# Kernel tuning notes

Hardware: AMD Instinct MI355X
Metric: run time of the kernel (lower is better)

The kernel has to match this reference:

```python
import jax, jax.numpy as jnp
import numpy as np

H = 1024       # hidden_size
I = 1024       # intermediate_size
E = 16         # num_experts
K = 4          # experts_per_token
LIMIT = 7.0    # swiglu_limit
ALPHA = 1.702  # swiglu alpha
EPS = 1e-5     # rmsnorm eps


def setup_inputs() -> dict:
    key = jax.random.key(0)
    ks = jax.random.split(key, 8)
    x = jax.random.normal(ks[0], (2, 512, H), dtype=jnp.float32)
    norm_scale = jnp.ones((H,), dtype=jnp.float32)
    wg = jax.random.normal(ks[1], (H, E), dtype=jnp.float32) * 0.02
    bg = jax.random.normal(ks[2], (E,), dtype=jnp.float32) * 0.02
    w1 = jax.random.normal(ks[3], (E, H, 2 * I), dtype=jnp.float32) * 0.02
    b1 = jax.random.normal(ks[4], (E, 2 * I), dtype=jnp.float32) * 0.02
    w2 = jax.random.normal(ks[5], (E, I, H), dtype=jnp.float32) * 0.02
    b2 = jax.random.normal(ks[6], (E, H), dtype=jnp.float32) * 0.02
    return {"x": x, "norm_scale": norm_scale, "wg": wg, "bg": bg,
            "w1": w1, "b1": b1, "w2": w2, "b2": b2}


def reference(x, norm_scale, wg, bg, w1, b1, w2, b2):
    shape = x.shape
    xf = x.reshape(-1, shape[-1])                                   # [T, H]
    # RMSNorm (float32 math)
    xn = xf * jax.lax.rsqrt(jnp.mean(xf * xf, axis=-1, keepdims=True) + EPS) * norm_scale
    # router logits + top-k with softmax over selected logits
    logits = xn @ wg + bg                                           # [T, E]
    vals, idx = jax.lax.top_k(logits, K)                            # [T, K]
    gates = jax.nn.softmax(vals, axis=-1)                           # [T, K]
    # dense [T, E] gate matrix (exactly equivalent to gather/scatter grouped GEMM)
    gate_full = jnp.einsum('tke,tk->te', jax.nn.one_hot(idx, E, dtype=gates.dtype), gates)
    # expert FFN 1 + fused swiglu (interleaved gate/linear pairs)
    h = jnp.einsum('th,ehd->etd', xn, w1) + b1[:, None, :]          # [E, T, 2I]
    a = jnp.minimum(h[..., ::2], LIMIT)                             # gate branch
    b = jnp.clip(h[..., 1::2], -LIMIT, LIMIT)                       # linear branch
    s = a * jax.nn.sigmoid(ALPHA * a) * (b + 1.0)                   # [E, T, I]
    # expert FFN 2; gamma (gate) scales the full epilogue incl. bias
    y = jnp.einsum('eti,eih->eth', s, w2) + b2[:, None, :]          # [E, T, H]
    t = jnp.einsum('eth,te->th', y, gate_full)                      # scatter-combine
    return x + t.reshape(shape)
```

## Files before the change

### kernel.cpp

```cpp
#include <hip/hip_runtime.h>

#define NH 1024
#define NI2 2048
#define NI 1024
#define NE 16
#define NT 1024

static constexpr float LIMITF = 7.0f;
static constexpr float ALPHAF = 1.702f;
static constexpr float EPSF = 1e-5f;

typedef short bf16x8 __attribute__((ext_vector_type(8)));
typedef float f32x4 __attribute__((ext_vector_type(4)));

__device__ __forceinline__ unsigned short f2bf(float f) {
  unsigned int u = __builtin_bit_cast(unsigned int, f);
  u = (u + 0x7FFFu + ((u >> 16) & 1u)) >> 16;
  return (unsigned short)u;
}

__global__ __launch_bounds__(256) void k_init(const float* __restrict__ x,
                                              float* __restrict__ out) {
  int i = blockIdx.x * 256 + threadIdx.x;
  reinterpret_cast<float4*>(out)[i] = reinterpret_cast<const float4*>(x)[i];
}

__global__ __launch_bounds__(256) void k_norm_router(
    const float* __restrict__ x, const float* __restrict__ nsc,
    const float* __restrict__ wg, const float* __restrict__ bg,
    unsigned short* __restrict__ xn, int* __restrict__ topk_idx,
    float* __restrict__ topk_gate, int* __restrict__ counts) {
  int t = blockIdx.x;
  int tid = threadIdx.x;
  int wave = tid >> 6, lane = tid & 63;

  float4 v = reinterpret_cast<const float4*>(x + (size_t)t * NH)[tid];
  float ss = v.x * v.x + v.y * v.y + v.z * v.z + v.w * v.w;
  for (int off = 32; off; off >>= 1) ss += __shfl_xor(ss, off);

  __shared__ float red[4];
  __shared__ float redl[4][16];
  __shared__ float logits_s[16];
  if (lane == 0) red[wave] = ss;
  __syncthreads();
  float tot = red[0] + red[1] + red[2] + red[3];
  float r = rsqrtf(tot * (1.0f / NH) + EPSF);

  float4 sc = reinterpret_cast<const float4*>(nsc)[tid];
  float xv[4];
  xv[0] = v.x * r * sc.x;
  xv[1] = v.y * r * sc.y;
  xv[2] = v.z * r * sc.z;
  xv[3] = v.w * r * sc.w;

  ushort4 o;
  o.x = f2bf(xv[0]); o.y = f2bf(xv[1]); o.z = f2bf(xv[2]); o.w = f2bf(xv[3]);
  reinterpret_cast<ushort4*>(xn + (size_t)t * NH)[tid] = o;

  float acc[16];
#pragma unroll
  for (int e = 0; e < 16; e++) acc[e] = 0.f;
  int hbase = tid * 4;
#pragma unroll
  for (int i = 0; i < 4; i++) {
    const float4* wr = reinterpret_cast<const float4*>(wg + (size_t)(hbase + i) * NE);
#pragma unroll
    for (int j = 0; j < 4; j++) {
      float4 w = wr[j];
      acc[j * 4 + 0] += xv[i] * w.x;
      acc[j * 4 + 1] += xv[i] * w.y;
      acc[j * 4 + 2] += xv[i] * w.z;
      acc[j * 4 + 3] += xv[i] * w.w;
    }
  }
#pragma unroll
  for (int e = 0; e < 16; e++)
    for (int off = 32; off; off >>= 1) acc[e] += __shfl_xor(acc[e], off);
  if (lane == 0) {
#pragma unroll
    for (int e = 0; e < 16; e++) redl[wave][e] = acc[e];
  }
  __syncthreads();
  if (tid < 16)
    logits_s[tid] = redl[0][tid] + redl[1][tid] + redl[2][tid] + redl[3][tid] + bg[tid];
  __syncthreads();

  if (tid == 0) {
    float vals[16];
#pragma unroll
    for (int e = 0; e < 16; e++) vals[e] = logits_s[e];
    int sel[4]; float sv[4];
    unsigned used = 0;
    for (int k = 0; k < 4; k++) {
      float best = -1e30f; int bi = 0;
      for (int e = 0; e < 16; e++) {
        if (!((used >> e) & 1u) && vals[e] > best) { best = vals[e]; bi = e; }
      }
      used |= 1u << bi; sel[k] = bi; sv[k] = best;
    }
    float g[4], ssum = 0.f;
    for (int k = 0; k < 4; k++) { g[k] = __expf(sv[k] - sv[0]); ssum += g[k]; }
    for (int k = 0; k < 4; k++) {
      topk_idx[t * 4 + k] = sel[k];
      topk_gate[t * 4 + k] = g[k] / ssum;
      atomicAdd(&counts[sel[k]], 1);
    }
  }
}

__global__ void k_scan(const int* __restrict__ counts, int* __restrict__ offsets,
                       int* __restrict__ cursor) {
  if (blockIdx.x == 0 && threadIdx.x == 0) {
    int o = 0;
    for (int e = 0; e < NE; e++) { offsets[e] = o; cursor[e] = o; o += counts[e]; }
  }
}

__global__ __launch_bounds__(256) void k_fill(const int* __restrict__ topk_idx,
                                              const float* __restrict__ topk_gate,
                                              int* __restrict__ cursor,
                                              int* __restrict__ rows_tok,
                                              float* __restrict__ rows_gate) {
  int idx = blockIdx.x * 256 + threadIdx.x;
  if (idx >= NT * 4) return;
  int e = topk_idx[idx];
  int slot = atomicAdd(&cursor[e], 1);
  rows_tok[slot] = idx >> 2;
  rows_gate[slot] = topk_gate[idx];
}

__global__ __launch_bounds__(256) void k_ffn1(
    const unsigned short* __restrict__ xn, const float* __restrict__ w1,
    const float* __restrict__ b1, const int* __restrict__ counts,
    const int* __restrict__ offsets, const int* __restrict__ rows_tok,
    unsigned short* __restrict__ s_buf) {
  int e = blockIdx.y;
  int cnt = counts[e];
  int m0 = blockIdx.z * 32;
  if (m0 >= cnt) return;
  int rowbase = offsets[e] + m0;
  int mcount = min(32, cnt - m0);
  int n0 = blockIdx.x * 64;
  int tid = threadIdx.x;

  __shared__ int tok_s[32];
  __shared__ __align__(16) unsigned short lds_a[32 * 32];
  __shared__ unsigned int lds_b[64 * 17];

  if (tid < 32) tok_s[tid] = rows_tok[rowbase + min(tid, mcount - 1)];
  __syncthreads();

  const int wave = tid >> 6, lane = tid & 63;
  const int quad = lane >> 4, l16 = lane & 15;
  const int m16 = (wave & 1) * 16;
  const int nw = (wave >> 1) * 32;

  f32x4 acc0 = {0.f, 0.f, 0.f, 0.f}, acc1 = {0.f, 0.f, 0.f, 0.f};

  const float* w1e = w1 + (size_t)e * NH * NI2 + n0;
  const int ar = tid >> 3, ac = (tid & 7) * 4;
  const int bn = tid & 63, bk0 = (tid >> 6) * 2;

  for (int k0 = 0; k0 < NH; k0 += 32) {
    uint2 av = *reinterpret_cast<const uint2*>(xn + (size_t)tok_s[ar] * NH + k0 + ac);
    *reinterpret_cast<uint2*>(&lds_a[ar * 32 + ac]) = av;
#pragma unroll
    for (int it = 0; it < 4; it++) {
      int kk = bk0 + it * 8;
      float f0 = w1e[(size_t)(k0 + kk) * NI2 + bn];
      float f1 = w1e[(size_t)(k0 + kk + 1) * NI2 + bn];
      lds_b[bn * 17 + (kk >> 1)] =
          (unsigned int)f2bf(f0) | ((unsigned int)f2bf(f1) << 16);
    }
    __syncthreads();
    bf16x8 a = *reinterpret_cast<const bf16x8*>(&lds_a[(m16 + l16) * 32 + quad * 8]);
    const unsigned int* bp0 = &lds_b[(nw + l16) * 17 + quad * 4];
    uint4 t0; t0.x = bp0[0]; t0.y = bp0[1]; t0.z = bp0[2]; t0.w = bp0[3];
    acc0 = __builtin_amdgcn_mfma_f32_16x16x32_bf16(
        a, __builtin_bit_cast(bf16x8, t0), acc0, 0, 0, 0);
    const unsigned int* bp1 = &lds_b[(nw + 16 + l16) * 17 + quad * 4];
    uint4 t1; t1.x = bp1[0]; t1.y = bp1[1]; t1.z = bp1[2]; t1.w = bp1[3];
    acc1 = __builtin_amdgcn_mfma_f32_16x16x32_bf16(
        a, __builtin_bit_cast(bf16x8, t1), acc1, 0, 0, 0);
    __syncthreads();
  }

  const float* b1e = b1 + (size_t)e * NI2 + n0;
  int parity = l16 & 1;
#pragma unroll
  for (int s2 = 0; s2 < 2; s2++) {
    f32x4 acc = s2 ? acc1 : acc0;
    int ncol = nw + s2 * 16 + l16;
    float bias = b1e[ncol];
#pragma unroll
    for (int r2 = 0; r2 < 4; r2++) {
      float v = acc[r2] + bias;
      float p = __shfl_xor(v, 1);
      int m = m16 + quad * 4 + r2;
      if (!parity && m < mcount) {
        float aa = fminf(v, LIMITF);
        float bb = fminf(fmaxf(p, -LIMITF), LIMITF);
        float sig = 1.0f / (1.0f + __expf(-ALPHAF * aa));
        float sval = aa * sig * (bb + 1.0f);
        s_buf[(size_t)(rowbase + m) * NI + ((n0 + ncol) >> 1)] = f2bf(sval);
      }
    }
  }
}

__global__ __launch_bounds__(256) void k_ffn2(
    const unsigned short* __restrict__ s_buf, const float* __restrict__ w2,
    const float* __restrict__ b2, const int* __restrict__ counts,
    const int* __restrict__ offsets, const int* __restrict__ rows_tok,
    const float* __restrict__ rows_gate, float* __restrict__ out) {
  int e = blockIdx.y;
  int cnt = counts[e];
  int m0 = blockIdx.z * 32;
  if (m0 >= cnt) return;
  int rowbase = offsets[e] + m0;
  int mcount = min(32, cnt - m0);
  int n0 = blockIdx.x * 64;
  int tid = threadIdx.x;

  __shared__ int tok_s[32];
  __shared__ float gate_s[32];
  __shared__ __align__(16) unsigned short lds_a[32 * 32];
  __shared__ unsigned int lds_b[64 * 17];

  if (tid < 32) {
    int rr = rowbase + min(tid, mcount - 1);
    tok_s[tid] = rows_tok[rr];
    gate_s[tid] = rows_gate[rr];
  }
  __syncthreads();

  const int wave = tid >> 6, lane = tid & 63;
  const int quad = lane >> 4, l16 = lane & 15;
  const int m16 = (wave & 1) * 16;
  const int nw = (wave >> 1) * 32;

  f32x4 acc0 = {0.f, 0.f, 0.f, 0.f}, acc1 = {0.f, 0.f, 0.f, 0.f};

  const float* w2e = w2 + (size_t)e * NI * NH + n0;
  const int ar = tid >> 3, ac = (tid & 7) * 4;
  const int bn = tid & 63, bk0 = (tid >> 6) * 2;

  for (int k0 = 0; k0 < NI; k0 += 32) {
    int arow = rowbase + min(ar, mcount - 1);
    uint2 av = *reinterpret_cast<const uint2*>(s_buf + (size_t)arow * NI + k0 + ac);
    *reinterpret_cast<uint2*>(&lds_a[ar * 32 + ac]) = av;
#pragma unroll
    for (int it = 0; it < 4; it++) {
      int kk = bk0 + it * 8;
      float f0 = w2e[(size_t)(k0 + kk) * NH + bn];
      float f1 = w2e[(size_t)(k0 + kk + 1) * NH + bn];
      lds_b[bn * 17 + (kk >> 1)] =
          (unsigned int)f2bf(f0) | ((unsigned int)f2bf(f1) << 16);
    }
    __syncthreads();
    bf16x8 a = *reinterpret_cast<const bf16x8*>(&lds_a[(m16 + l16) * 32 + quad * 8]);
    const unsigned int* bp0 = &lds_b[(nw + l16) * 17 + quad * 4];
    uint4 t0; t0.x = bp0[0]; t0.y = bp0[1]; t0.z = bp0[2]; t0.w = bp0[3];
    acc0 = __builtin_amdgcn_mfma_f32_16x16x32_bf16(
        a, __builtin_bit_cast(bf16x8, t0), acc0, 0, 0, 0);
    const unsigned int* bp1 = &lds_b[(nw + 16 + l16) * 17 + quad * 4];
    uint4 t1; t1.x = bp1[0]; t1.y = bp1[1]; t1.z = bp1[2]; t1.w = bp1[3];
    acc1 = __builtin_amdgcn_mfma_f32_16x16x32_bf16(
        a, __builtin_bit_cast(bf16x8, t1), acc1, 0, 0, 0);
    __syncthreads();
  }

  const float* b2e = b2 + (size_t)e * NH + n0;
#pragma unroll
  for (int s2 = 0; s2 < 2; s2++) {
    f32x4 acc = s2 ? acc1 : acc0;
    int ncol = nw + s2 * 16 + l16;
    float bias = b2e[ncol];
#pragma unroll
    for (int r2 = 0; r2 < 4; r2++) {
      int m = m16 + quad * 4 + r2;
      if (m < mcount) {
        float y = acc[r2] + bias;
        atomicAdd(&out[(size_t)tok_s[m] * NH + n0 + ncol], gate_s[m] * y);
      }
    }
  }
}

extern "C" void kernel_launch(void* const* d_in, const int* in_sizes, int n_in,
                              void* d_out, int out_size, void* d_ws, size_t ws_size,
                              hipStream_t stream) {
  const float* x   = (const float*)d_in[0];
  const float* nsc = (const float*)d_in[1];
  const float* wg  = (const float*)d_in[2];
  const float* bg  = (const float*)d_in[3];
  const float* w1  = (const float*)d_in[4];
  const float* b1  = (const float*)d_in[5];
  const float* w2  = (const float*)d_in[6];
  const float* b2  = (const float*)d_in[7];
  float* out = (float*)d_out;
  char* ws = (char*)d_ws;

  int*   counts    = (int*)(ws + 0);
  int*   offsets   = (int*)(ws + 64);
  int*   cursor    = (int*)(ws + 128);
  int*   topk_idx  = (int*)(ws + 1024);
  float* topk_gate = (float*)(ws + 1024 + 16384);
  int*   rows_tok  = (int*)(ws + 1024 + 32768);
  float* rows_gate = (float*)(ws + 1024 + 49152);
  unsigned short* xn    = (unsigned short*)(ws + 131072);
  unsigned short* s_buf = (unsigned short*)(ws + 4 * 1024 * 1024);

  hipMemsetAsync(ws, 0, 256, stream);
  k_init<<<NT * NH / 1024, 256, 0, stream>>>(x, out);
  k_norm_router<<<NT, 256, 0, stream>>>(x, nsc, wg, bg, xn, topk_idx, topk_gate,
                                        counts);
  k_scan<<<1, 64, 0, stream>>>(counts, offsets, cursor);
  k_fill<<<16, 256, 0, stream>>>(topk_idx, topk_gate, cursor, rows_tok, rows_gate);
  k_ffn1<<<dim3(NI2 / 64, NE, 32), 256, 0, stream>>>(xn, w1, b1, counts, offsets,
                                                     rows_tok, s_buf);
  k_ffn2<<<dim3(NH / 64, NE, 32), 256, 0, stream>>>(s_buf, w2, b2, counts, offsets,
                                                    rows_tok, rows_gate, out);
}
```

Measured before the change: 484.3 us.

## Keep full-K weight column strip resident in LDS and loop over all expert rows

Each block now converts a 32-column strip of the expert weight (full K) to bf16 once into 64KB of LDS. It then loops over every token row of that expert, using 32x32x16 MFMAs with A operands read straight from global memory. Before, each 32-row tile re-read and re-converted the fp32 weights, so weight traffic scaled with the number of row tiles. The cost is far fewer blocks (NE x 64 or NE x 32), large LDS use that limits occupancy, and A loads without LDS staging.

```diff
diff --git a/kernel.cpp b/kernel.cpp
--- a/kernel.cpp
+++ b/kernel.cpp
@@ -11,7 +11,7 @@
 static constexpr float EPSF = 1e-5f;
 
 typedef short bf16x8 __attribute__((ext_vector_type(8)));
-typedef float f32x4 __attribute__((ext_vector_type(4)));
+typedef float f32x16 __attribute__((ext_vector_type(16)));
 
 __device__ __forceinline__ unsigned short f2bf(float f) {
   unsigned int u = __builtin_bit_cast(unsigned int, f);
@@ -136,73 +136,90 @@
     unsigned short* __restrict__ s_buf) {
   int e = blockIdx.y;
   int cnt = counts[e];
-  int m0 = blockIdx.z * 32;
-  if (m0 >= cnt) return;
-  int rowbase = offsets[e] + m0;
-  int mcount = min(32, cnt - m0);
-  int n0 = blockIdx.x * 64;
+  if (cnt == 0) return;
+  int n0 = blockIdx.x * 32;
+  int rowbase = offsets[e];
   int tid = threadIdx.x;
 
-  __shared__ int tok_s[32];
-  __shared__ __align__(16) unsigned short lds_a[32 * 32];
-  __shared__ unsigned int lds_b[64 * 17];
-
-  if (tid < 32) tok_s[tid] = rows_tok[rowbase + min(tid, mcount - 1)];
-  __syncthreads();
-
-  const int wave = tid >> 6, lane = tid & 63;
-  const int quad = lane >> 4, l16 = lane & 15;
-  const int m16 = (wave & 1) * 16;
-  const int nw = (wave >> 1) * 32;
-
-  f32x4 acc0 = {0.f, 0.f, 0.f, 0.f}, acc1 = {0.f, 0.f, 0.f, 0.f};
-
-  const float* w1e = w1 + (size_t)e * NH * NI2 + n0;
-  const int ar = tid >> 3, ac = (tid & 7) * 4;
-  const int bn = tid & 63, bk0 = (tid >> 6) * 2;
-
-  for (int k0 = 0; k0 < NH; k0 += 32) {
-    uint2 av = *reinterpret_cast<const uint2*>(xn + (size_t)tok_s[ar] * NH + k0 + ac);
-    *reinterpret_cast<uint2*>(&lds_a[ar * 32 + ac]) = av;
-#pragma unroll
-    for (int it = 0; it < 4; it++) {
-      int kk = bk0 + it * 8;
-      float f0 = w1e[(size_t)(k0 + kk) * NI2 + bn];
-      float f1 = w1e[(size_t)(k0 + kk + 1) * NI2 + bn];
-      lds_b[bn * 17 + (kk >> 1)] =
-          (unsigned int)f2bf(f0) | ((unsigned int)f2bf(f1) << 16);
-    }
-    __syncthreads();
-    bf16x8 a = *reinterpret_cast<const bf16x8*>(&lds_a[(m16 + l16) * 32 + quad * 8]);
-    const unsigned int* bp0 = &lds_b[(nw + l16) * 17 + quad * 4];
-    uint4 t0; t0.x = bp0[0]; t0.y = bp0[1]; t0.z = bp0[2]; t0.w = bp0[3];
-    acc0 = __builtin_amdgcn_mfma_f32_16x16x32_bf16(
-        a, __builtin_bit_cast(bf16x8, t0), acc0, 0, 0, 0);
-    const unsigned int* bp1 = &lds_b[(nw + 16 + l16) * 17 + quad * 4];
-    uint4 t1; t1.x = bp1[0]; t1.y = bp1[1]; t1.z = bp1[2]; t1.w = bp1[3];
-    acc1 = __builtin_amdgcn_mfma_f32_16x16x32_bf16(
-        a, __builtin_bit_cast(bf16x8, t1), acc1, 0, 0, 0);
-    __syncthreads();
-  }
-
-  const float* b1e = b1 + (size_t)e * NI2 + n0;
-  int parity = l16 & 1;
-#pragma unroll
-  for (int s2 = 0; s2 < 2; s2++) {
-    f32x4 acc = s2 ? acc1 : acc0;
-    int ncol = nw + s2 * 16 + l16;
-    float bias = b1e[ncol];
-#pragma unroll
-    for (int r2 = 0; r2 < 4; r2++) {
-      float v = acc[r2] + bias;
-      float p = __shfl_xor(v, 1);
-      int m = m16 + quad * 4 + r2;
-      if (!parity && m < mcount) {
-        float aa = fminf(v, LIMITF);
-        float bb = fminf(fmaxf(p, -LIMITF), LIMITF);
-        float sig = 1.0f / (1.0f + __expf(-ALPHAF * aa));
-        float sval = aa * sig * (bb + 1.0f);
-        s_buf[(size_t)(rowbase + m) * NI + ((n0 + ncol) >> 1)] = f2bf(sval);
+  __shared__ __align__(16) unsigned short lds_b[128 * 32 * 8];
+
+  const float* w1e = w1 + (size_t)e * (NH * NI2) + n0;
+  {
+    int col = tid & 31;
+    int kc8 = tid >> 5;
+    for (int p = 0; p < 16; p++) {
+      int kb = p * 64 + kc8 * 8;
+      float f[8];
+#pragma unroll
+      for (int j = 0; j < 8; j++) f[j] = w1e[(size_t)(kb + j) * NI2 + col];
+      unsigned int pk[4];
+#pragma unroll
+      for (int j = 0; j < 4; j++)
+        pk[j] = (unsigned)f2bf(f[2 * j]) | ((unsigned)f2bf(f[2 * j + 1]) << 16);
+      *reinterpret_cast<uint4*>(&lds_b[(size_t)((kb >> 3) * 32 + col) * 8]) =
+          *reinterpret_cast<const uint4*>(pk);
+    }
+  }
+  __syncthreads();
+
+  int lane = tid & 63;
+  int wave = tid >> 6;
+  int lrow = lane & 31;
+  int khalf = lane >> 5;
+
+  float bias = b1[(size_t)e * NI2 + n0 + lrow];
+  int parity = lrow & 1;
+
+  for (int m0 = 0; m0 < cnt; m0 += 256) {
+    int tb0 = m0 + wave * 32;
+    int tb1 = m0 + 128 + wave * 32;
+    int tok0 = rows_tok[rowbase + min(tb0 + lrow, cnt - 1)];
+    const unsigned short* a0p = xn + (size_t)tok0 * NH + khalf * 8;
+
+    f32x16 acc0 = {0.f,0.f,0.f,0.f,0.f,0.f,0.f,0.f,0.f,0.f,0.f,0.f,0.f,0.f,0.f,0.f};
+    f32x16 acc1 = {0.f,0.f,0.f,0.f,0.f,0.f,0.f,0.f,0.f,0.f,0.f,0.f,0.f,0.f,0.f,0.f};
+    bool dual = (m0 + 128) < cnt;
+
+    if (dual) {
+      int tok1 = rows_tok[rowbase + min(tb1 + lrow, cnt - 1)];
+      const unsigned short* a1p = xn + (size_t)tok1 * NH + khalf * 8;
+#pragma unroll 4
+      for (int k2 = 0; k2 < 64; k2++) {
+        bf16x8 av0 = *reinterpret_cast<const bf16x8*>(a0p + k2 * 16);
+        bf16x8 av1 = *reinterpret_cast<const bf16x8*>(a1p + k2 * 16);
+        bf16x8 bv = *reinterpret_cast<const bf16x8*>(
+            &lds_b[(size_t)((k2 * 2 + khalf) * 32 + lrow) * 8]);
+        acc0 = __builtin_amdgcn_mfma_f32_32x32x16_bf16(av0, bv, acc0, 0, 0, 0);
+        acc1 = __builtin_amdgcn_mfma_f32_32x32x16_bf16(av1, bv, acc1, 0, 0, 0);
+      }
+    } else {
+#pragma unroll 4
+      for (int k2 = 0; k2 < 64; k2++) {
+        bf16x8 av0 = *reinterpret_cast<const bf16x8*>(a0p + k2 * 16);
+        bf16x8 bv = *reinterpret_cast<const bf16x8*>(
+            &lds_b[(size_t)((k2 * 2 + khalf) * 32 + lrow) * 8]);
+        acc0 = __builtin_amdgcn_mfma_f32_32x32x16_bf16(av0, bv, acc0, 0, 0, 0);
+      }
+    }
+
+#pragma unroll
+    for (int t2 = 0; t2 < 2; t2++) {
+      if (t2 == 1 && !dual) break;
+      f32x16 acc = t2 ? acc1 : acc0;
+      int tb = t2 ? tb1 : tb0;
+#pragma unroll
+      for (int reg = 0; reg < 16; reg++) {
+        float v = acc[reg] + bias;
+        float p = __shfl_xor(v, 1);
+        int row = (reg & 3) + 8 * (reg >> 2) + 4 * khalf;
+        int m = tb + row;
+        if (!parity && m < cnt) {
+          float aa = fminf(v, LIMITF);
+          float bb = fminf(fmaxf(p, -LIMITF), LIMITF);
+          float sig = 1.0f / (1.0f + __expf(-ALPHAF * aa));
+          float sval = aa * sig * (bb + 1.0f);
+          s_buf[(size_t)(rowbase + m) * NI + ((n0 + lrow) >> 1)] = f2bf(sval);
+        }
       }
     }
   }
@@ -215,73 +232,86 @@
     const float* __restrict__ rows_gate, float* __restrict__ out) {
   int e = blockIdx.y;
   int cnt = counts[e];
-  int m0 = blockIdx.z * 32;
-  if (m0 >= cnt) return;
-  int rowbase = offsets[e] + m0;
-  int mcount = min(32, cnt - m0);
-  int n0 = blockIdx.x * 64;
+  if (cnt == 0) return;
+  int n0 = blockIdx.x * 32;
+  int rowbase = offsets[e];
   int tid = threadIdx.x;
 
-  __shared__ int tok_s[32];
-  __shared__ float gate_s[32];
-  __shared__ __align__(16) unsigned short lds_a[32 * 32];
-  __shared__ unsigned int lds_b[64 * 17];
-
-  if (tid < 32) {
-    int rr = rowbase + min(tid, mcount - 1);
-    tok_s[tid] = rows_tok[rr];
-    gate_s[tid] = rows_gate[rr];
-  }
-  __syncthreads();
-
-  const int wave = tid >> 6, lane = tid & 63;
-  const int quad = lane >> 4, l16 = lane & 15;
-  const int m16 = (wave & 1) * 16;
-  const int nw = (wave >> 1) * 32;
-
-  f32x4 acc0 = {0.f, 0.f, 0.f, 0.f}, acc1 = {0.f, 0.f, 0.f, 0.f};
-
-  const float* w2e = w2 + (size_t)e * NI * NH + n0;
-  const int ar = tid >> 3, ac = (tid & 7) * 4;
-  const int bn = tid & 63, bk0 = (tid >> 6) * 2;
-
-  for (int k0 = 0; k0 < NI; k0 += 32) {
-    int arow = rowbase + min(ar, mcount - 1);
-    uint2 av = *reinterpret_cast<const uint2*>(s_buf + (size_t)arow * NI + k0 + ac);
-    *reinterpret_cast<uint2*>(&lds_a[ar * 32 + ac]) = av;
-#pragma unroll
-    for (int it = 0; it < 4; it++) {
-      int kk = bk0 + it * 8;
-      float f0 = w2e[(size_t)(k0 + kk) * NH + bn];
-      float f1 = w2e[(size_t)(k0 + kk + 1) * NH + bn];
-      lds_b[bn * 17 + (kk >> 1)] =
-          (unsigned int)f2bf(f0) | ((unsigned int)f2bf(f1) << 16);
-    }
-    __syncthreads();
-    bf16x8 a = *reinterpret_cast<const bf16x8*>(&lds_a[(m16 + l16) * 32 + quad * 8]);
-    const unsigned int* bp0 = &lds_b[(nw + l16) * 17 + quad * 4];
-    uint4 t0; t0.x = bp0[0]; t0.y = bp0[1]; t0.z = bp0[2]; t0.w = bp0[3];
-    acc0 = __builtin_amdgcn_mfma_f32_16x16x32_bf16(
-        a, __builtin_bit_cast(bf16x8, t0), acc0, 0, 0, 0);
-    const unsigned int* bp1 = &lds_b[(nw + 16 + l16) * 17 + quad * 4];
-    uint4 t1; t1.x = bp1[0]; t1.y = bp1[1]; t1.z = bp1[2]; t1.w = bp1[3];
-    acc1 = __builtin_amdgcn_mfma_f32_16x16x32_bf16(
-        a, __builtin_bit_cast(bf16x8, t1), acc1, 0, 0, 0);
-    __syncthreads();
-  }
-
-  const float* b2e = b2 + (size_t)e * NH + n0;
-#pragma unroll
-  for (int s2 = 0; s2 < 2; s2++) {
-    f32x4 acc = s2 ? acc1 : acc0;
-    int ncol = nw + s2 * 16 + l16;
-    float bias = b2e[ncol];
-#pragma unroll
-    for (int r2 = 0; r2 < 4; r2++) {
-      int m = m16 + quad * 4 + r2;
-      if (m < mcount) {
-        float y = acc[r2] + bias;
-        atomicAdd(&out[(size_t)tok_s[m] * NH + n0 + ncol], gate_s[m] * y);
+  __shared__ __align__(16) unsigned short lds_b[128 * 32 * 8];
+
+  const float* w2e = w2 + (size_t)e * (NI * NH) + n0;
+  {
+    int col = tid & 31;
+    int kc8 = tid >> 5;
+    for (int p = 0; p < 16; p++) {
+      int kb = p * 64 + kc8 * 8;
+      float f[8];
+#pragma unroll
+      for (int j = 0; j < 8; j++) f[j] = w2e[(size_t)(kb + j) * NH + col];
+      unsigned int pk[4];
+#pragma unroll
+      for (int j = 0; j < 4; j++)
+        pk[j] = (unsigned)f2bf(f[2 * j]) | ((unsigned)f2bf(f[2 * j + 1]) << 16);
+      *reinterpret_cast<uint4*>(&lds_b[(size_t)((kb >> 3) * 32 + col) * 8]) =
+          *reinterpret_cast<const uint4*>(pk);
+    }
+  }
+  __syncthreads();
+
+  int lane = tid & 63;
+  int wave = tid >> 6;
+  int lrow = lane & 31;
+  int khalf = lane >> 5;
+
+  float b2v = b2[(size_t)e * NH + n0 + lrow];
+
+  for (int m0 = 0; m0 < cnt; m0 += 256) {
+    int tb0 = m0 + wave * 32;
+    int tb1 = m0 + 128 + wave * 32;
+    int r0 = rowbase + min(tb0 + lrow, cnt - 1);
+    const unsigned short* a0p = s_buf + (size_t)r0 * NI + khalf * 8;
+
+    f32x16 acc0 = {0.f,0.f,0.f,0.f,0.f,0.f,0.f,0.f,0.f,0.f,0.f,0.f,0.f,0.f,0.f,0.f};
+    f32x16 acc1 = {0.f,0.f,0.f,0.f,0.f,0.f,0.f,0.f,0.f,0.f,0.f,0.f,0.f,0.f,0.f,0.f};
+    bool dual = (m0 + 128) < cnt;
+
+    if (dual) {
+      int r1 = rowbase + min(tb1 + lrow, cnt - 1);
+      const unsigned short* a1p = s_buf + (size_t)r1 * NI + khalf * 8;
+#pragma unroll 4
+      for (int k2 = 0; k2 < 64; k2++) {
+        bf16x8 av0 = *reinterpret_cast<const bf16x8*>(a0p + k2 * 16);
+        bf16x8 av1 = *reinterpret_cast<const bf16x8*>(a1p + k2 * 16);
+        bf16x8 bv = *reinterpret_cast<const bf16x8*>(
+            &lds_b[(size_t)((k2 * 2 + khalf) * 32 + lrow) * 8]);
+        acc0 = __builtin_amdgcn_mfma_f32_32x32x16_bf16(av0, bv, acc0, 0, 0, 0);
+        acc1 = __builtin_amdgcn_mfma_f32_32x32x16_bf16(av1, bv, acc1, 0, 0, 0);
+      }
+    } else {
+#pragma unroll 4
+      for (int k2 = 0; k2 < 64; k2++) {
+        bf16x8 av0 = *reinterpret_cast<const bf16x8*>(a0p + k2 * 16);
+        bf16x8 bv = *reinterpret_cast<const bf16x8*>(
+            &lds_b[(size_t)((k2 * 2 + khalf) * 32 + lrow) * 8]);
+        acc0 = __builtin_amdgcn_mfma_f32_32x32x16_bf16(av0, bv, acc0, 0, 0, 0);
+      }
+    }
+
+#pragma unroll
+    for (int t2 = 0; t2 < 2; t2++) {
+      if (t2 == 1 && !dual) break;
+      f32x16 acc = t2 ? acc1 : acc0;
+      int tb = t2 ? tb1 : tb0;
+#pragma unroll
+      for (int reg = 0; reg < 16; reg++) {
+        int row = (reg & 3) + 8 * (reg >> 2) + 4 * khalf;
+        int m = tb + row;
+        if (m < cnt) {
+          int rr = rowbase + m;
+          int tok = rows_tok[rr];
+          float g = rows_gate[rr];
+          atomicAdd(&out[(size_t)tok * NH + n0 + lrow], g * (acc[reg] + b2v));
+        }
       }
     }
   }
@@ -317,8 +347,8 @@
                                         counts);
   k_scan<<<1, 64, 0, stream>>>(counts, offsets, cursor);
   k_fill<<<16, 256, 0, stream>>>(topk_idx, topk_gate, cursor, rows_tok, rows_gate);
-  k_ffn1<<<dim3(NI2 / 64, NE, 32), 256, 0, stream>>>(xn, w1, b1, counts, offsets,
-                                                     rows_tok, s_buf);
-  k_ffn2<<<dim3(NH / 64, NE, 32), 256, 0, stream>>>(s_buf, w2, b2, counts, offsets,
-                                                    rows_tok, rows_gate, out);
-}
+  k_ffn1<<<dim3(NI2 / 32, NE), 256, 0, stream>>>(xn, w1, b1, counts, offsets,
+                                                 rows_tok, s_buf);
+  k_ffn2<<<dim3(NH / 32, NE), 256, 0, stream>>>(s_buf, w2, b2, counts, offsets,
+                                                rows_tok, rows_gate, out);
+}
```

New measurement: 453.3 us. 6.4% less time.
